# Kernel optimization log

Hardware: AMD Instinct MI355X
Metric: run time of the kernel (lower is better)

## Reference

```python
import jax, jax.numpy as jnp
import numpy as np

G_NUM, K_DEG = 3, 3  # grid intervals, spline order (module defaults)
LN_EPS = 1e-5


def _bspline_basis(x, grid, k):
    """Cox-de Boor B-spline basis. x: [N, D], grid: [D, G+2k+1] -> [N, D, G+k]."""
    xg = x[:, :, None]                      # [N, D, 1]
    g = grid[None, :, :]                    # [1, D, M]
    B = ((xg >= g[..., :-1]) & (xg < g[..., 1:])).astype(x.dtype)  # degree 0
    for d in range(1, k + 1):
        left = (xg - g[..., :-(d + 1)]) / (g[..., d:-1] - g[..., :-(d + 1)])
        right = (g[..., d + 1:] - xg) / (g[..., d + 1:] - g[..., 1:-d])
        B = left * B[..., :-1] + right * B[..., 1:]
    return B                                # [N, D, G+k]


def _kan_layer(x, grid, coef, scale_base, scale_sp, node_scale, node_bias):
    # spline branch: fold per-edge scale_sp into coef, contract basis without
    # materializing the [N, in, out] per-edge tensor
    basis = _bspline_basis(x, grid, K_DEG)              # [N, in, G+k]
    coef_eff = coef * scale_sp[..., None]               # [in, out, G+k]
    y = jnp.einsum('nib,iob->no', basis, coef_eff)      # spline sum over edges
    y = y + jax.nn.silu(x) @ scale_base                 # residual base function
    return node_scale * y + node_bias                   # per-node affine


def setup_inputs() -> dict:
    key = jax.random.key(0)
    ks = jax.random.split(key, 12)
    B, S = 16, 1024
    D0, D1, D2 = 256, 512, 256
    nb = G_NUM + K_DEG  # num basis fns = 6
    h = 2.0 / G_NUM
    knots = np.arange(-K_DEG, G_NUM + K_DEG + 1) * h - 1.0  # [G+2k+1]=10, range [-3,3]
    grid1 = jnp.asarray(np.tile(knots, (D0, 1)), jnp.float32)
    grid2 = jnp.asarray(np.tile(knots, (D1, 1)), jnp.float32)
    inp = {
        'x': jax.random.normal(ks[0], (B, S, D0), jnp.float32),
        'grid1': grid1,
        'coef1': jax.random.normal(ks[1], (D0, D1, nb), jnp.float32) * 0.1,
        'scale_base1': jax.random.normal(ks[2], (D0, D1), jnp.float32) / np.sqrt(D0),
        'scale_sp1': jnp.ones((D0, D1), jnp.float32),
        'node_scale1': jnp.ones((D1,), jnp.float32),
        'node_bias1': jnp.zeros((D1,), jnp.float32),
        'grid2': grid2,
        'coef2': jax.random.normal(ks[3], (D1, D2, nb), jnp.float32) * 0.1,
        'scale_base2': jax.random.normal(ks[4], (D1, D2), jnp.float32) / np.sqrt(D1),
        'scale_sp2': jnp.ones((D1, D2), jnp.float32),
        'node_scale2': jnp.ones((D2,), jnp.float32),
        'node_bias2': jnp.zeros((D2,), jnp.float32),
        'ln_gamma': jnp.ones((D2,), jnp.float32),
        'ln_beta': jnp.zeros((D2,), jnp.float32),
    }
    return inp


def reference(x, grid1, coef1, scale_base1, scale_sp1, node_scale1, node_bias1,
              grid2, coef2, scale_base2, scale_sp2, node_scale2, node_bias2,
              ln_gamma, ln_beta):
    b, s, d = x.shape
    residual = x  # start_dim == final_dim -> residual path active
    h = x.reshape(-1, d)
    h = _kan_layer(h, grid1, coef1, scale_base1, scale_sp1, node_scale1, node_bias1)
    h = _kan_layer(h, grid2, coef2, scale_base2, scale_sp2, node_scale2, node_bias2)
    h = h.reshape(b, s, -1)
    h = h + residual
    # LayerNorm over last dim
    mu = jnp.mean(h, axis=-1, keepdims=True)
    var = jnp.mean((h - mu) ** 2, axis=-1, keepdims=True)
    h = (h - mu) * jax.lax.rsqrt(var + LN_EPS) * ln_gamma + ln_beta
    # torch nn.GELU default is exact (erf) variant
    return jax.nn.gelu(h, approximate=False)
```

## Files before the change

kernel.cpp:

```cpp
#include <hip/hip_runtime.h>
#include <cstdint>
#include <cstddef>

using f16   = _Float16;
using half4 = __attribute__((ext_vector_type(4))) _Float16;
using half8 = __attribute__((ext_vector_type(8))) _Float16;
using f32x4 = __attribute__((ext_vector_type(4))) float;
using ull   = unsigned long long;

#define DINL __device__ __forceinline__

DINL void gload_lds16(const void* gptr, void* lptr) {
  __builtin_amdgcn_global_load_lds(
      reinterpret_cast<const __attribute__((address_space(1))) uint32_t*>(
          reinterpret_cast<uintptr_t>(gptr)),
      reinterpret_cast<__attribute__((address_space(3))) uint32_t*>(
          reinterpret_cast<uintptr_t>(lptr)),
      16, 0, 0);
}

DINL unsigned pkh(float a, float b) {
  unsigned short ha = __builtin_bit_cast(unsigned short, (f16)a);
  unsigned short hb = __builtin_bit_cast(unsigned short, (f16)b);
  return (unsigned)ha | ((unsigned)hb << 16);
}

struct U4 { unsigned x, y, z, w; };

DINL U4 expand_pack(float x) {
  float xs = (x + 3.0f) * 1.5f;
  float mf = floorf(xs);
  int   m  = (int)mf;
  float u = xs - mf, u2 = u * u, u3 = u2 * u, um = 1.0f - u;
  float p3 = u3 * (1.0f / 6.0f);
  float p2 = (1.0f + 3.0f * (u + u2 - u3)) * (1.0f / 6.0f);
  float p1 = (4.0f - 6.0f * u2 + 3.0f * u3) * (1.0f / 6.0f);
  float p0 = um * um * um * (1.0f / 6.0f);
  ull P = (ull)pkh(p0, p1) | ((ull)pkh(p2, p3) << 32);
  if ((unsigned)m > 8u) P = 0;
  int s    = m * 16 - 48;
  int sneg = min(63, max(0, -s));
  int spos = min(63, max(0, s));
  int shi2 = min(63, max(0, s - 64));
  ull rlo = (s < 0) ? (P >> sneg) : ((s < 64) ? (P << spos) : 0ull);
  ull rhi = (s < 0) ? 0ull
                    : ((s < 64) ? ((P >> (63 - spos)) >> 1) : (P << shi2));
  float sil = x / (1.0f + __expf(-x));
  U4 r;
  r.x = (unsigned)rlo;
  r.y = (unsigned)(rlo >> 32);
  r.z = (unsigned)rhi;
  r.w = pkh(sil, 0.0f);
  return r;
}

__global__ __launch_bounds__(256)
void prep_w_kernel(const float* __restrict__ coef, const float* __restrict__ ssp,
                   const float* __restrict__ sb, f16* __restrict__ Wt,
                   int Din, int Dout) {
  int idx = blockIdx.x * 256 + threadIdx.x;
  if (idx >= Din * Dout) return;
  int n = idx / Din;
  int d = idx - n * Din;
  float s = ssp[(size_t)d * Dout + n];
  const float* c = coef + ((size_t)d * Dout + n) * 6;
  half8 wv;
#pragma unroll
  for (int b = 0; b < 6; ++b) wv[b] = (f16)(c[b] * s);
  wv[6] = (f16)sb[(size_t)d * Dout + n];
  wv[7] = (f16)0.0f;
  int dp = (d & ~7) | ((d & 7) ^ (n & 7));
  *reinterpret_cast<half8*>(Wt + ((size_t)n * Din + dp) * 8) = wv;
}

template <bool BIAS, typename TIN, typename TOUT>
__global__ __launch_bounds__(256, 2)
void kan_gemm(const TIN* __restrict__ X, int ldx,
              const f16* __restrict__ Wt, int ldw,
              const float* __restrict__ nscale, const float* __restrict__ nbias,
              int N, TOUT* __restrict__ Out, int nsteps) {
  __shared__ alignas(16) f16 A0[64 * 64];
  __shared__ alignas(16) f16 A1[64 * 64];
  __shared__ alignas(16) f16 B0[256 * 64];
  __shared__ alignas(16) f16 B1[256 * 64];

  const int tid  = threadIdx.x;
  const int w    = tid >> 6;
  const int lane = tid & 63;
  const int l15  = lane & 15, l7 = lane & 7, hi = lane >> 4;
  const int m0   = blockIdx.y * 64;
  const int n0   = blockIdx.x * 256;
  const int dim0 = blockIdx.z * (nsteps * 8);
  TOUT* outz = Out + (size_t)blockIdx.z * ((size_t)gridDim.y * 64) * N;

  const int ar = tid >> 3, ad = tid & 7;
  const TIN* asrc0 = X + (size_t)(m0 + ar) * ldx + dim0 + ad;
  const TIN* asrc1 = asrc0 + (size_t)32 * ldx;
  const int aoff0 = ar * 64 + 8 * (ad ^ (ar & 7));
  const int aoff1 = aoff0 + 32 * 64;

  const f16* wsrc = Wt + (size_t)(n0 + (tid >> 3)) * ldw + (size_t)dim0 * 8 + (tid & 7) * 8;
  f16* const bdst = (f16*)nullptr;

  f32x4 acc[4][4] = {};

  auto stageB = [&](f16* buf, int k0) {
#pragma unroll
    for (int q = 0; q < 8; ++q)
      gload_lds16(wsrc + (size_t)q * 32 * ldw + k0, buf + tid * 8 + q * 2048);
  };

  auto compute = [&](const f16* bA, const f16* bB) {
    __builtin_amdgcn_s_setprio(1);
#pragma unroll
    for (int kk = 0; kk < 2; ++kk) {
      const int sl = kk * 4 + hi;
      half8 av[4], bv[4];
#pragma unroll
      for (int i = 0; i < 4; ++i)
        av[i] = *reinterpret_cast<const half8*>(
            bA + (i * 16 + l15) * 64 + 8 * (sl ^ l7));
#pragma unroll
      for (int j = 0; j < 4; ++j)
        bv[j] = *reinterpret_cast<const half8*>(
            bB + (w * 64 + j * 16 + l15) * 64 + 8 * (sl ^ l7));
#pragma unroll
      for (int i = 0; i < 4; ++i)
#pragma unroll
        for (int j = 0; j < 4; ++j)
          acc[i][j] = __builtin_amdgcn_mfma_f32_16x16x32_f16(av[i], bv[j], acc[i][j], 0, 0, 0);
    }
    __builtin_amdgcn_s_setprio(0);
  };

  auto writeA = [&](f16* buf, U4 e0, U4 e1) {
    *reinterpret_cast<U4*>(buf + aoff0) = e0;
    *reinterpret_cast<U4*>(buf + aoff1) = e1;
  };

  {
    float xa0 = (float)asrc0[0], xa1 = (float)asrc1[0];
    stageB(B0, 0);
    writeA(A0, expand_pack(xa0), expand_pack(xa1));
  }
  float xn0 = (float)asrc0[8], xn1 = (float)asrc1[8];
  __syncthreads();

  const int npairs = (nsteps - 2) >> 1;
  int k  = 64;
  int kd = 16;
  for (int p = 0; p < npairs; ++p) {
    stageB(B1, k);
    float xa0 = (float)asrc0[kd], xa1 = (float)asrc1[kd];
    compute(A0, B0);
    writeA(A1, expand_pack(xn0), expand_pack(xn1));
    __syncthreads();
    stageB(B0, k + 64);
    xn0 = (float)asrc0[kd + 8]; xn1 = (float)asrc1[kd + 8];
    compute(A1, B1);
    writeA(A0, expand_pack(xa0), expand_pack(xa1));
    __syncthreads();
    k  += 128;
    kd += 16;
  }

  stageB(B1, k);
  compute(A0, B0);
  writeA(A1, expand_pack(xn0), expand_pack(xn1));
  __syncthreads();
  compute(A1, B1);

#pragma unroll
  for (int j = 0; j < 4; ++j) {
    int col   = n0 + w * 64 + j * 16 + l15;
    float nsv = nscale[col];
    float nbv = BIAS ? nbias[col] : 0.0f;
#pragma unroll
    for (int i = 0; i < 4; ++i) {
      int rb = m0 + i * 16 + hi * 4;
#pragma unroll
      for (int r = 0; r < 4; ++r)
        outz[(size_t)(rb + r) * N + col] = (TOUT)(nsv * acc[i][j][r] + nbv);
    }
  }
}

__global__ __launch_bounds__(256)
void ln_gelu_kernel(const f16* __restrict__ P0, const f16* __restrict__ P1,
                    const float* __restrict__ X,  const float* __restrict__ nb2,
                    const float* __restrict__ gamma, const float* __restrict__ beta,
                    float* __restrict__ out, int rows) {
  int row  = blockIdx.x * 4 + (threadIdx.x >> 6);
  int lane = threadIdx.x & 63;
  if (row >= rows) return;
  const half4  a4 = *reinterpret_cast<const half4*>(P0 + (size_t)row * 256 + lane * 4);
  const half4  b4 = *reinterpret_cast<const half4*>(P1 + (size_t)row * 256 + lane * 4);
  const float4 xr = *reinterpret_cast<const float4*>(X  + (size_t)row * 256 + lane * 4);
  const float4 nb = *reinterpret_cast<const float4*>(nb2 + lane * 4);
  const float4 g  = *reinterpret_cast<const float4*>(gamma + lane * 4);
  const float4 be = *reinterpret_cast<const float4*>(beta + lane * 4);
  float h[4];
#pragma unroll
  for (int j = 0; j < 4; ++j)
    h[j] = (float)a4[j] + (float)b4[j] + (&nb.x)[j] + (&xr.x)[j];
  float s = h[0] + h[1] + h[2] + h[3];
#pragma unroll
  for (int o = 32; o >= 1; o >>= 1) s += __shfl_xor(s, o);
  float mu = s * (1.0f / 256.0f);
  float vs = 0.f;
#pragma unroll
  for (int j = 0; j < 4; ++j) { float d = h[j] - mu; vs += d * d; }
#pragma unroll
  for (int o = 32; o >= 1; o >>= 1) vs += __shfl_xor(vs, o);
  float inv = rsqrtf(vs * (1.0f / 256.0f) + 1e-5f);
  float o4[4];
#pragma unroll
  for (int j = 0; j < 4; ++j) {
    float v = (h[j] - mu) * inv * (&g.x)[j] + (&be.x)[j];
    o4[j] = 0.5f * v * (1.0f + erff(v * 0.70710678118654752f));
  }
  *reinterpret_cast<float4*>(out + (size_t)row * 256 + lane * 4) =
      make_float4(o4[0], o4[1], o4[2], o4[3]);
}

extern "C" void kernel_launch(void* const* d_in, const int* in_sizes, int n_in,
                              void* d_out, int out_size, void* d_ws, size_t ws_size,
                              hipStream_t stream) {
  (void)in_sizes; (void)n_in; (void)out_size; (void)ws_size;
  const float* x     = (const float*)d_in[0];
  const float* coef1 = (const float*)d_in[2];
  const float* sb1   = (const float*)d_in[3];
  const float* ssp1  = (const float*)d_in[4];
  const float* ns1   = (const float*)d_in[5];
  const float* nb1   = (const float*)d_in[6];
  const float* coef2 = (const float*)d_in[8];
  const float* sb2   = (const float*)d_in[9];
  const float* ssp2  = (const float*)d_in[10];
  const float* ns2   = (const float*)d_in[11];
  const float* nb2   = (const float*)d_in[12];
  const float* lgam  = (const float*)d_in[13];
  const float* lbet  = (const float*)d_in[14];
  float* out = (float*)d_out;

  const int Ntok = 16 * 1024;
  const int D0 = 256, D1 = 512, D2 = 256;

  char* ws    = (char*)d_ws;
  f16*  h1    = (f16*)ws;
  size_t off  = (size_t)Ntok * D1 * sizeof(f16);
  f16*  part  = (f16*)(ws + off);
  off += (size_t)2 * Ntok * D2 * sizeof(f16);
  f16* Wt1 = (f16*)(ws + off);
  off += (size_t)D1 * D0 * 8 * sizeof(f16);
  f16* Wt2 = (f16*)(ws + off);

  prep_w_kernel<<<(D0 * D1 + 255) / 256, 256, 0, stream>>>(coef1, ssp1, sb1, Wt1, D0, D1);
  prep_w_kernel<<<(D1 * D2 + 255) / 256, 256, 0, stream>>>(coef2, ssp2, sb2, Wt2, D1, D2);

  kan_gemm<true, float, f16><<<dim3(D1 / 256, Ntok / 64, 1), 256, 0, stream>>>(
      x, D0, Wt1, D0 * 8, ns1, nb1, D1, h1, D0 / 8);

  kan_gemm<false, f16, f16><<<dim3(D2 / 256, Ntok / 64, 2), 256, 0, stream>>>(
      h1, D1, Wt2, D1 * 8, ns2, nullptr, D2, part, D1 / 16);

  ln_gelu_kernel<<<Ntok / 4, 256, 0, stream>>>(
      part, part + (size_t)Ntok * D2, x, nb2, lgam, lbet, out, Ntok);
}
```

Measured before the change: 119.7 us.

## Split-K both KAN GEMMs, single-buffer LDS for higher occupancy

Layer-1 GEMM now splits its K dimension in two and writes two fp16 partial outputs. Layer-2 reads the sum of those two partials as its input and itself splits K four ways. LayerNorm then sums four partials. The LDS double buffers are collapsed to single buffers with extra barriers, and launch bounds rise to 3 blocks per CU. The aim is more blocks and higher occupancy. The cost is lost load/compute overlap, more partial-sum global traffic, and added fp16 rounding error in the partials.

```diff
diff --git a/kernel.cpp b/kernel.cpp
--- a/kernel.cpp
+++ b/kernel.cpp
@@ -73,16 +73,14 @@
   *reinterpret_cast<half8*>(Wt + ((size_t)n * Din + dp) * 8) = wv;
 }
 
-template <bool BIAS, typename TIN, typename TOUT>
-__global__ __launch_bounds__(256, 2)
-void kan_gemm(const TIN* __restrict__ X, int ldx,
+template <bool BIAS, int NSRC, typename TIN, typename TOUT>
+__global__ __launch_bounds__(256, 3)
+void kan_gemm(const TIN* __restrict__ X0, const TIN* __restrict__ X1, int ldx,
               const f16* __restrict__ Wt, int ldw,
               const float* __restrict__ nscale, const float* __restrict__ nbias,
               int N, TOUT* __restrict__ Out, int nsteps) {
-  __shared__ alignas(16) f16 A0[64 * 64];
-  __shared__ alignas(16) f16 A1[64 * 64];
-  __shared__ alignas(16) f16 B0[256 * 64];
-  __shared__ alignas(16) f16 B1[256 * 64];
+  __shared__ alignas(16) f16 AA[64 * 64];
+  __shared__ alignas(16) f16 BB[256 * 64];
 
   const int tid  = threadIdx.x;
   const int w    = tid >> 6;
@@ -94,23 +92,37 @@
   TOUT* outz = Out + (size_t)blockIdx.z * ((size_t)gridDim.y * 64) * N;
 
   const int ar = tid >> 3, ad = tid & 7;
-  const TIN* asrc0 = X + (size_t)(m0 + ar) * ldx + dim0 + ad;
-  const TIN* asrc1 = asrc0 + (size_t)32 * ldx;
+  const TIN* a0 = X0 + (size_t)(m0 + ar) * ldx + dim0 + ad;
+  const TIN* a1 = a0 + (size_t)32 * ldx;
+  const TIN* b0 = nullptr;
+  const TIN* b1 = nullptr;
+  if constexpr (NSRC == 2) {
+    b0 = X1 + (size_t)(m0 + ar) * ldx + dim0 + ad;
+    b1 = b0 + (size_t)32 * ldx;
+  }
   const int aoff0 = ar * 64 + 8 * (ad ^ (ar & 7));
   const int aoff1 = aoff0 + 32 * 64;
 
+  auto loadx = [&](int doff, float& u, float& v) {
+    u = (float)a0[doff];
+    v = (float)a1[doff];
+    if constexpr (NSRC == 2) {
+      u += (float)b0[doff];
+      v += (float)b1[doff];
+    }
+  };
+
   const f16* wsrc = Wt + (size_t)(n0 + (tid >> 3)) * ldw + (size_t)dim0 * 8 + (tid & 7) * 8;
-  f16* const bdst = (f16*)nullptr;
 
   f32x4 acc[4][4] = {};
 
-  auto stageB = [&](f16* buf, int k0) {
+  auto stageB = [&](int k0) {
 #pragma unroll
     for (int q = 0; q < 8; ++q)
-      gload_lds16(wsrc + (size_t)q * 32 * ldw + k0, buf + tid * 8 + q * 2048);
+      gload_lds16(wsrc + (size_t)q * 32 * ldw + k0, BB + tid * 8 + q * 2048);
   };
 
-  auto compute = [&](const f16* bA, const f16* bB) {
+  auto compute = [&]() {
     __builtin_amdgcn_s_setprio(1);
 #pragma unroll
     for (int kk = 0; kk < 2; ++kk) {
@@ -119,11 +131,11 @@
 #pragma unroll
       for (int i = 0; i < 4; ++i)
         av[i] = *reinterpret_cast<const half8*>(
-            bA + (i * 16 + l15) * 64 + 8 * (sl ^ l7));
+            AA + (i * 16 + l15) * 64 + 8 * (sl ^ l7));
 #pragma unroll
       for (int j = 0; j < 4; ++j)
         bv[j] = *reinterpret_cast<const half8*>(
-            bB + (w * 64 + j * 16 + l15) * 64 + 8 * (sl ^ l7));
+            BB + (w * 64 + j * 16 + l15) * 64 + 8 * (sl ^ l7));
 #pragma unroll
       for (int i = 0; i < 4; ++i)
 #pragma unroll
@@ -133,48 +145,39 @@
     __builtin_amdgcn_s_setprio(0);
   };
 
-  auto writeA = [&](f16* buf, U4 e0, U4 e1) {
-    *reinterpret_cast<U4*>(buf + aoff0) = e0;
-    *reinterpret_cast<U4*>(buf + aoff1) = e1;
-  };
-
   {
-    float xa0 = (float)asrc0[0], xa1 = (float)asrc1[0];
-    stageB(B0, 0);
-    writeA(A0, expand_pack(xa0), expand_pack(xa1));
-  }
-  float xn0 = (float)asrc0[8], xn1 = (float)asrc1[8];
-  __syncthreads();
-
-  const int npairs = (nsteps - 2) >> 1;
-  int k  = 64;
-  int kd = 16;
-  for (int p = 0; p < npairs; ++p) {
-    stageB(B1, k);
-    float xa0 = (float)asrc0[kd], xa1 = (float)asrc1[kd];
-    compute(A0, B0);
-    writeA(A1, expand_pack(xn0), expand_pack(xn1));
+    float xu, xv;
+    loadx(0, xu, xv);
+    stageB(0);
+    float yu0, yv0;
+    loadx(8, yu0, yv0);
+    U4 e0 = expand_pack(xu), e1 = expand_pack(xv);
+    *reinterpret_cast<U4*>(AA + aoff0) = e0;
+    *reinterpret_cast<U4*>(AA + aoff1) = e1;
     __syncthreads();
-    stageB(B0, k + 64);
-    xn0 = (float)asrc0[kd + 8]; xn1 = (float)asrc1[kd + 8];
-    compute(A1, B1);
-    writeA(A0, expand_pack(xa0), expand_pack(xa1));
-    __syncthreads();
-    k  += 128;
-    kd += 16;
-  }
-
-  stageB(B1, k);
-  compute(A0, B0);
-  writeA(A1, expand_pack(xn0), expand_pack(xn1));
-  __syncthreads();
-  compute(A1, B1);
+
+    float yu = yu0, yv = yv0;
+    for (int s = 0; s < nsteps - 1; ++s) {
+      compute();
+      __syncthreads();
+      stageB((s + 1) * 64);
+      const int nd = (s + 2 < nsteps ? s + 2 : nsteps - 1) * 8;
+      float zu, zv;
+      loadx(nd, zu, zv);
+      U4 e2 = expand_pack(yu), e3 = expand_pack(yv);
+      *reinterpret_cast<U4*>(AA + aoff0) = e2;
+      *reinterpret_cast<U4*>(AA + aoff1) = e3;
+      yu = zu; yv = zv;
+      __syncthreads();
+    }
+    compute();
+  }
 
 #pragma unroll
   for (int j = 0; j < 4; ++j) {
     int col   = n0 + w * 64 + j * 16 + l15;
     float nsv = nscale[col];
-    float nbv = BIAS ? nbias[col] : 0.0f;
+    float nbv = (BIAS && blockIdx.z == 0) ? nbias[col] : 0.0f;
 #pragma unroll
     for (int i = 0; i < 4; ++i) {
       int rb = m0 + i * 16 + hi * 4;
@@ -186,23 +189,26 @@
 }
 
 __global__ __launch_bounds__(256)
-void ln_gelu_kernel(const f16* __restrict__ P0, const f16* __restrict__ P1,
+void ln_gelu_kernel(const f16* __restrict__ P, size_t zstride,
                     const float* __restrict__ X,  const float* __restrict__ nb2,
                     const float* __restrict__ gamma, const float* __restrict__ beta,
                     float* __restrict__ out, int rows) {
   int row  = blockIdx.x * 4 + (threadIdx.x >> 6);
   int lane = threadIdx.x & 63;
   if (row >= rows) return;
-  const half4  a4 = *reinterpret_cast<const half4*>(P0 + (size_t)row * 256 + lane * 4);
-  const half4  b4 = *reinterpret_cast<const half4*>(P1 + (size_t)row * 256 + lane * 4);
-  const float4 xr = *reinterpret_cast<const float4*>(X  + (size_t)row * 256 + lane * 4);
+  const size_t base = (size_t)row * 256 + lane * 4;
+  const float4 xr = *reinterpret_cast<const float4*>(X + base);
   const float4 nb = *reinterpret_cast<const float4*>(nb2 + lane * 4);
   const float4 g  = *reinterpret_cast<const float4*>(gamma + lane * 4);
   const float4 be = *reinterpret_cast<const float4*>(beta + lane * 4);
-  float h[4];
-#pragma unroll
-  for (int j = 0; j < 4; ++j)
-    h[j] = (float)a4[j] + (float)b4[j] + (&nb.x)[j] + (&xr.x)[j];
+  float h[4] = { (&nb.x)[0] + (&xr.x)[0], (&nb.x)[1] + (&xr.x)[1],
+                 (&nb.x)[2] + (&xr.x)[2], (&nb.x)[3] + (&xr.x)[3] };
+#pragma unroll
+  for (int z = 0; z < 4; ++z) {
+    const half4 p4 = *reinterpret_cast<const half4*>(P + z * zstride + base);
+#pragma unroll
+    for (int j = 0; j < 4; ++j) h[j] += (float)p4[j];
+  }
   float s = h[0] + h[1] + h[2] + h[3];
 #pragma unroll
   for (int o = 32; o >= 1; o >>= 1) s += __shfl_xor(s, o);
@@ -245,11 +251,13 @@
   const int Ntok = 16 * 1024;
   const int D0 = 256, D1 = 512, D2 = 256;
 
-  char* ws    = (char*)d_ws;
-  f16*  h1    = (f16*)ws;
-  size_t off  = (size_t)Ntok * D1 * sizeof(f16);
-  f16*  part  = (f16*)(ws + off);
-  off += (size_t)2 * Ntok * D2 * sizeof(f16);
+  char* ws     = (char*)d_ws;
+  f16*  h1p    = (f16*)ws;
+  size_t h1z   = (size_t)Ntok * D1;
+  size_t off   = 2 * h1z * sizeof(f16);
+  f16*  part   = (f16*)(ws + off);
+  size_t partz = (size_t)Ntok * D2;
+  off += 4 * partz * sizeof(f16);
   f16* Wt1 = (f16*)(ws + off);
   off += (size_t)D1 * D0 * 8 * sizeof(f16);
   f16* Wt2 = (f16*)(ws + off);
@@ -257,12 +265,12 @@
   prep_w_kernel<<<(D0 * D1 + 255) / 256, 256, 0, stream>>>(coef1, ssp1, sb1, Wt1, D0, D1);
   prep_w_kernel<<<(D1 * D2 + 255) / 256, 256, 0, stream>>>(coef2, ssp2, sb2, Wt2, D1, D2);
 
-  kan_gemm<true, float, f16><<<dim3(D1 / 256, Ntok / 64, 1), 256, 0, stream>>>(
-      x, D0, Wt1, D0 * 8, ns1, nb1, D1, h1, D0 / 8);
-
-  kan_gemm<false, f16, f16><<<dim3(D2 / 256, Ntok / 64, 2), 256, 0, stream>>>(
-      h1, D1, Wt2, D1 * 8, ns2, nullptr, D2, part, D1 / 16);
+  kan_gemm<true, 1, float, f16><<<dim3(D1 / 256, Ntok / 64, 2), 256, 0, stream>>>(
+      x, nullptr, D0, Wt1, D0 * 8, ns1, nb1, D1, h1p, D0 / 16);
+
+  kan_gemm<false, 2, f16, f16><<<dim3(D2 / 256, Ntok / 64, 4), 256, 0, stream>>>(
+      h1p, h1p + h1z, D1, Wt2, D1 * 8, ns2, nullptr, D2, part, D1 / 32);
 
   ln_gelu_kernel<<<Ntok / 4, 256, 0, stream>>>(
-      part, part + (size_t)Ntok * D2, x, nb2, lgam, lbet, out, Ntok);
-}
+      part, partz, x, nb2, lgam, lbet, out, Ntok);
+}
```

Measured after the change: 131.1 us. 1.09x slower.
